# Kernel tuning notes

Hardware: AMD Instinct MI355X
Metric: run time of the kernel (lower is better)

Reference implementation:

```python
import jax, jax.numpy as jnp
import numpy as np

B, S, D, H, DH, R = 8, 2048, 1024, 16, 64, 32
ALPHA, BETA, GAMMA = 0.2, 0.1, 0.1


def setup_inputs() -> dict:
    key = jax.random.key(0)
    ks = jax.random.split(key, 5)
    x = jax.random.normal(ks[0], (B, S, D), jnp.float32)
    q = jax.random.normal(ks[1], (B, S, H, DH), jnp.float32)
    k = jax.random.normal(ks[2], (B, S, H, DH), jnp.float32)
    v_value = jax.random.normal(ks[3], (B, S, D), jnp.float32)
    # reentry_proj weight (orthogonal init approximated by scaled gaussian)
    W = jax.random.normal(ks[4], (D, D), jnp.float32) * np.float32(np.sqrt(0.5 / D))
    return {"x": x, "q": q, "k": k, "v_value": v_value, "W": W}


def _normalize(t):
    return t / (jnp.linalg.norm(t, axis=-1, keepdims=True) + 1e-6)


def reference(x, q, k, v_value, W):
    Bz, Sl, Dm = x.shape
    qf = q.reshape(Bz, Sl, Dm).transpose(1, 0, 2)        # (S, B, D)
    kf = k.reshape(Bz, Sl, Dm).transpose(1, 0, 2)        # (S, B, D)
    vf = v_value.transpose(1, 0, 2)                      # (S, B, D)
    U0 = jnp.zeros((Bz, R, Dm), x.dtype)
    V0 = jnp.zeros((Bz, R, Dm), x.dtype)

    def step(carry, inp):
        U, V = carry
        q_t, k_t, v_t = inp                              # each (B, D)
        U = (1.0 - ALPHA) * U + ALPHA * _normalize(q_t)[:, None, :]
        V = (1.0 - ALPHA) * V + ALPHA * _normalize(k_t)[:, None, :]
        # y_t = (U^T V) v_t, computed factorized: never materialize dim x dim
        s = jnp.einsum('brd,bd->br', V, v_t)             # (B, R)
        y = jnp.einsum('brd,br->bd', U, s)               # (B, D)
        n = jnp.maximum(jnp.linalg.norm(y, axis=-1, keepdims=True), 1e-6)
        y = y / (1.0 + BETA * (n - 1.0))                 # homeostasis
        fb = GAMMA * (y @ W.T)                           # reentry projection
        return (U, V), fb

    (_, _), fbs = jax.lax.scan(step, (U0, V0), (qf, kf, vf))
    return x + fbs.transpose(1, 0, 2)                    # (B, S, D)
```

## Files before the change

kernel.cpp:

```cpp
#include <hip/hip_runtime.h>
#include <hip/hip_bf16.h>
#include <cstdint>
#include <cstddef>

#define B_ 8
#define S_ 2048
#define D_ 1024
#define RFAC 32.0f
#define ALPHA 0.2f
#define BETA 0.1f
#define GAMMA 0.1f
#define KW 32
#define TB 64
#define PF_ 8

typedef float f32x4_t __attribute__((ext_vector_type(4)));
typedef short bf16x8_t __attribute__((ext_vector_type(8)));

__device__ __forceinline__ unsigned short f2bf(float f) {
    unsigned u = __float_as_uint(f);
    u = (u + 0x7fffu + ((u >> 16) & 1u)) >> 16;
    return (unsigned short)u;
}
__device__ __forceinline__ float bf2f(unsigned short h) {
    return __uint_as_float(((unsigned)h) << 16);
}

__global__ __launch_bounds__(256) void norms_k(const float* __restrict__ q,
                                               const float* __restrict__ k,
                                               float* __restrict__ rnq,
                                               float* __restrict__ rnk) {
    int row  = blockIdx.x * 4 + (threadIdx.x >> 6);
    int lane = threadIdx.x & 63;
    const float4* qr = (const float4*)(q + (size_t)row * D_);
    const float4* kr = (const float4*)(k + (size_t)row * D_);
    float sq = 0.f, sk = 0.f;
#pragma unroll
    for (int j = 0; j < 4; ++j) {
        float4 a = qr[lane + 64 * j];
        float4 b = kr[lane + 64 * j];
        sq += a.x * a.x + a.y * a.y + a.z * a.z + a.w * a.w;
        sk += b.x * b.x + b.y * b.y + b.z * b.z + b.w * b.w;
    }
#pragma unroll
    for (int off = 32; off > 0; off >>= 1) {
        sq += __shfl_xor(sq, off, 64);
        sk += __shfl_xor(sk, off, 64);
    }
    if (lane == 0) {
        rnq[row] = ALPHA / (sqrtf(sq) + 1e-6f);
        rnk[row] = ALPHA / (sqrtf(sk) + 1e-6f);
    }
}

__global__ __launch_bounds__(256) void wconv_k(const float* __restrict__ W,
                                               unsigned short* __restrict__ Wb) {
    int i = blockIdx.x * 256 + threadIdx.x;
    float4 w = ((const float4*)W)[i];
    ushort4 o;
    o.x = f2bf(w.x); o.y = f2bf(w.y); o.z = f2bf(w.z); o.w = f2bf(w.w);
    ((ushort4*)Wb)[i] = o;
}

__global__ __launch_bounds__(256) void ema_coef_k(const float* __restrict__ q,
                                                  const float* __restrict__ kk,
                                                  const float* __restrict__ rnq,
                                                  const float* __restrict__ rnk,
                                                  const float* __restrict__ vv,
                                                  unsigned short* __restrict__ Ub,
                                                  float* __restrict__ coef) {
    __shared__ float sm[TB * 8];
    const int chunks = S_ / TB;
    int b  = blockIdx.x / chunks;
    int t0 = (blockIdx.x % chunks) * TB;
    int ts = t0 - KW; if (ts < 0) ts = 0;
    int tid = threadIdx.x;
    int lane = tid & 63, wave = tid >> 6;
    size_t bbase = (size_t)b * S_ * D_ + tid * 4;
    const float* qp = q + bbase;
    const float* kp = kk + bbase;
    const float* vp = vv + bbase;
    unsigned short* up = Ub + bbase;
    const float* rq = rnq + b * S_;
    const float* rk = rnk + b * S_;

    float4 pq[PF_], pk[PF_], pv[PF_];
    float paq[PF_], pak[PF_];
#pragma unroll
    for (int j = 0; j < PF_; ++j) {
        size_t o = (size_t)(ts + j) * D_;
        pq[j] = *(const float4*)(qp + o);
        pk[j] = *(const float4*)(kp + o);
        paq[j] = rq[ts + j];
        pak[j] = rk[ts + j];
        if (ts + j >= t0) pv[j] = *(const float4*)(vp + o);
    }
    float u0 = 0.f, u1 = 0.f, u2 = 0.f, u3 = 0.f;
    float v0 = 0.f, v1 = 0.f, v2 = 0.f, v3 = 0.f;
    const float om = 1.f - ALPHA;
    const int NI = t0 + TB - ts;
    const int tend = t0 + TB;
    for (int g = 0; g < NI; g += PF_) {
#pragma unroll
        for (int j = 0; j < PF_; ++j) {
            int t = ts + g + j;
            float aq = paq[j], ak = pak[j];
            u0 = om * u0 + aq * pq[j].x; u1 = om * u1 + aq * pq[j].y;
            u2 = om * u2 + aq * pq[j].z; u3 = om * u3 + aq * pq[j].w;
            v0 = om * v0 + ak * pk[j].x; v1 = om * v1 + ak * pk[j].y;
            v2 = om * v2 + ak * pk[j].z; v3 = om * v3 + ak * pk[j].w;
            if (t >= t0) {
                float uu = u0 * u0 + u1 * u1 + u2 * u2 + u3 * u3;
                float sd = v0 * pv[j].x + v1 * pv[j].y + v2 * pv[j].z + v3 * pv[j].w;
#pragma unroll
                for (int off = 32; off > 0; off >>= 1) {
                    uu += __shfl_xor(uu, off, 64);
                    sd += __shfl_xor(sd, off, 64);
                }
                if (lane == 0) {
                    sm[(t - t0) * 8 + wave * 2 + 0] = uu;
                    sm[(t - t0) * 8 + wave * 2 + 1] = sd;
                }
                ushort4 us;
                us.x = f2bf(u0); us.y = f2bf(u1); us.z = f2bf(u2); us.w = f2bf(u3);
                *(ushort4*)(up + (size_t)t * D_) = us;
            }
            int tf = t + PF_;
            int tc = tf < tend ? tf : tend - 1;
            size_t o2 = (size_t)tc * D_;
            pq[j] = *(const float4*)(qp + o2);
            pk[j] = *(const float4*)(kp + o2);
            paq[j] = rq[tc];
            pak[j] = rk[tc];
            if (tf >= t0) pv[j] = *(const float4*)(vp + o2);
        }
    }
    __syncthreads();
    if (tid < TB) {
        float uu = sm[tid * 8 + 0] + sm[tid * 8 + 2] + sm[tid * 8 + 4] + sm[tid * 8 + 6];
        float sd = sm[tid * 8 + 1] + sm[tid * 8 + 3] + sm[tid * 8 + 5] + sm[tid * 8 + 7];
        float nrm = RFAC * fabsf(sd) * sqrtf(uu);
        float n = fmaxf(nrm, 1e-6f);
        coef[b * S_ + t0 + tid] = GAMMA * RFAC * sd / (1.f + BETA * (n - 1.f));
    }
}

#define BM 256
#define BN 256
#define BK 64
#define NT (D_ / BK)

__global__ __launch_bounds__(512, 2) void gemm_k(const unsigned short* __restrict__ A,
                                                 const unsigned short* __restrict__ Bw,
                                                 const float* __restrict__ coef,
                                                 const float* __restrict__ x,
                                                 float* __restrict__ out) {
    const int N = D_, K = D_;
    __shared__ unsigned short lds[2 * 2 * BM * BK];
    int bid = blockIdx.x;
    int swz = (bid & 7) * 32 + (bid >> 3);
    int tm = swz >> 2, tn = swz & 3;
    int m0 = tm * BM, n0 = tn * BN;
    int tid = threadIdx.x;
    int lane = tid & 63;
    int wid = tid >> 6;
    int wm = wid >> 2, wn = wid & 3;
    int lr = lane & 15, lg = lane >> 4;

    f32x4_t acc[8][4];
#pragma unroll
    for (int i = 0; i < 8; ++i)
#pragma unroll
        for (int j = 0; j < 4; ++j)
            acc[i][j] = (f32x4_t){0.f, 0.f, 0.f, 0.f};

#define STAGE_HALF(buf, kt, h)                                                        \
    {                                                                                 \
        int isB = (h) >> 1;                                                           \
        const unsigned short* Gp =                                                    \
            (isB ? Bw + (size_t)n0 * K : A + (size_t)m0 * K) + (size_t)(kt) * BK;     \
        unsigned short* Lp = lds + (buf) * 32768 + isB * 16384;                       \
        _Pragma("unroll")                                                             \
        for (int i = 0; i < 2; ++i) {                                                 \
            int c = i * 512 + tid;                \
            int row = ((h) & 1) * 128 + (c >> 3);                                     \
            int cl = c & 7;                                                           \
            int gc = cl ^ (row & 7);                   \
            __builtin_amdgcn_global_load_lds(                                         \
                (const __attribute__((address_space(1))) void*)(Gp + (size_t)row * K + gc * 8), \
                (__attribute__((address_space(3))) void*)((char*)Lp + (((((h)&1)*128 + (c>>3)) * 8 + cl) * 16)), \
                16, 0, 0);                                                            \
        }                                                                             \
    }
#define STAGE_TILE(buf, kt)                                                           \
    STAGE_HALF(buf, kt, 0); STAGE_HALF(buf, kt, 1);                                   \
    STAGE_HALF(buf, kt, 2); STAGE_HALF(buf, kt, 3);

    STAGE_TILE(0, 0);
    STAGE_TILE(1, 1);

    for (int t = 0; t < NT; ++t) {
        if (t == NT - 1) asm volatile("s_waitcnt vmcnt(0)" ::: "memory");
        else             asm volatile("s_waitcnt vmcnt(8)" ::: "memory");
        __builtin_amdgcn_s_barrier();
        const unsigned short* La = lds + (t & 1) * 32768;
        const unsigned short* Lb = La + 16384;
        bf16x8_t bfrag[4][2];
#pragma unroll
        for (int p = 0; p < 4; ++p) {
            if (p == 0) {
#pragma unroll
                for (int ni = 0; ni < 4; ++ni)
#pragma unroll
                    for (int kkk = 0; kkk < 2; ++kkk) {
                        int row = wn * 64 + ni * 16 + lr;
                        int ch = (kkk * 4 + lg) ^ (row & 7);
                        bfrag[ni][kkk] = *(const bf16x8_t*)(Lb + (row * 8 + ch) * 8);
                    }
            }
            bf16x8_t afrag[2][2];
#pragma unroll
            for (int qq = 0; qq < 2; ++qq)
#pragma unroll
                for (int kkk = 0; kkk < 2; ++kkk) {
                    int row = wm * 128 + p * 32 + qq * 16 + lr;
                    int ch = (kkk * 4 + lg) ^ (row & 7);
                    afrag[qq][kkk] = *(const bf16x8_t*)(La + (row * 8 + ch) * 8);
                }
            asm volatile("s_waitcnt lgkmcnt(0)" ::: "memory");
            __builtin_amdgcn_sched_barrier(0);
            __builtin_amdgcn_s_setprio(1);
#pragma unroll
            for (int qq = 0; qq < 2; ++qq)
#pragma unroll
                for (int ni = 0; ni < 4; ++ni)
#pragma unroll
                    for (int kkk = 0; kkk < 2; ++kkk)
                        acc[p * 2 + qq][ni] = __builtin_amdgcn_mfma_f32_16x16x32_bf16(
                            afrag[qq][kkk], bfrag[ni][kkk], acc[p * 2 + qq][ni], 0, 0, 0);
            __builtin_amdgcn_s_setprio(0);
            __builtin_amdgcn_s_barrier();
        }
        if (t + 2 < NT) { STAGE_TILE((t & 1), t + 2); }
    }
#undef STAGE_TILE
#undef STAGE_HALF

#pragma unroll
    for (int mi = 0; mi < 8; ++mi) {
#pragma unroll
        for (int i = 0; i < 4; ++i) {
            int m = m0 + wm * 128 + mi * 16 + lg * 4 + i;
            float cf = coef[m];
#pragma unroll
            for (int ni = 0; ni < 4; ++ni) {
                int n = n0 + wn * 64 + ni * 16 + lr;
                size_t idx = (size_t)m * N + n;
                out[idx] = x[idx] + cf * acc[mi][ni][i];
            }
        }
    }
}

extern "C" void kernel_launch(void* const* d_in, const int* in_sizes, int n_in,
                              void* d_out, int out_size, void* d_ws, size_t ws_size,
                              hipStream_t stream) {
    const float* x  = (const float*)d_in[0];
    const float* q  = (const float*)d_in[1];
    const float* k  = (const float*)d_in[2];
    const float* vv = (const float*)d_in[3];
    const float* W  = (const float*)d_in[4];
    float* out = (float*)d_out;

    const size_t M = (size_t)B_ * S_;
    char* ws = (char*)d_ws;
    unsigned short* Ub = (unsigned short*)ws;
    unsigned short* Wb = (unsigned short*)(ws + M * D_ * 2);
    float* coef = (float*)(ws + M * D_ * 2 + (size_t)D_ * D_ * 2);
    float* rnq  = coef + M;
    float* rnk  = rnq + M;
    size_t needed = M * D_ * 2 + (size_t)D_ * D_ * 2 + 3 * M * 4;
    if (ws_size < needed) return;

    norms_k<<<dim3(M / 4), dim3(256), 0, stream>>>(q, k, rnq, rnk);
    wconv_k<<<dim3((D_ * D_) / 1024), dim3(256), 0, stream>>>(W, Wb);
    ema_coef_k<<<dim3(B_ * (S_ / TB)), dim3(256), 0, stream>>>(q, k, rnq, rnk, vv, Ub, coef);
    gemm_k<<<dim3((M / BM) * (D_ / BN)), dim3(512), 0, stream>>>(Ub, Wb, coef, x, out);
}
```

Baseline: 129.4 us.

## Fuse row norms into EMA kernel and shrink GEMM tiles to 128x128

Removes the separate norms kernel by computing q/k row norms inside the EMA scan via wave shuffles plus a block-level LDS reduction with a __syncthreads per timestep. This saves one full read of q and k from global memory and one launch, but it adds a block barrier on every step of the serial recurrence, including the warm-up steps. The GEMM also moves from 256x256 tiles with 512 threads to 128x128 tiles with 256 threads and 4x4 accumulators per wave. That gives more blocks and lower register pressure, at the cost of less data reuse per tile.

```diff
diff --git a/kernel.cpp b/kernel.cpp
--- a/kernel.cpp
+++ b/kernel.cpp
@@ -26,33 +26,6 @@
     return __uint_as_float(((unsigned)h) << 16);
 }
 
-__global__ __launch_bounds__(256) void norms_k(const float* __restrict__ q,
-                                               const float* __restrict__ k,
-                                               float* __restrict__ rnq,
-                                               float* __restrict__ rnk) {
-    int row  = blockIdx.x * 4 + (threadIdx.x >> 6);
-    int lane = threadIdx.x & 63;
-    const float4* qr = (const float4*)(q + (size_t)row * D_);
-    const float4* kr = (const float4*)(k + (size_t)row * D_);
-    float sq = 0.f, sk = 0.f;
-#pragma unroll
-    for (int j = 0; j < 4; ++j) {
-        float4 a = qr[lane + 64 * j];
-        float4 b = kr[lane + 64 * j];
-        sq += a.x * a.x + a.y * a.y + a.z * a.z + a.w * a.w;
-        sk += b.x * b.x + b.y * b.y + b.z * b.z + b.w * b.w;
-    }
-#pragma unroll
-    for (int off = 32; off > 0; off >>= 1) {
-        sq += __shfl_xor(sq, off, 64);
-        sk += __shfl_xor(sk, off, 64);
-    }
-    if (lane == 0) {
-        rnq[row] = ALPHA / (sqrtf(sq) + 1e-6f);
-        rnk[row] = ALPHA / (sqrtf(sk) + 1e-6f);
-    }
-}
-
 __global__ __launch_bounds__(256) void wconv_k(const float* __restrict__ W,
                                                unsigned short* __restrict__ Wb) {
     int i = blockIdx.x * 256 + threadIdx.x;
@@ -62,14 +35,13 @@
     ((ushort4*)Wb)[i] = o;
 }
 
-__global__ __launch_bounds__(256) void ema_coef_k(const float* __restrict__ q,
-                                                  const float* __restrict__ kk,
-                                                  const float* __restrict__ rnq,
-                                                  const float* __restrict__ rnk,
-                                                  const float* __restrict__ vv,
-                                                  unsigned short* __restrict__ Ub,
-                                                  float* __restrict__ coef) {
-    __shared__ float sm[TB * 8];
+__global__ __launch_bounds__(256) void ema_fused_k(const float* __restrict__ q,
+                                                   const float* __restrict__ kk,
+                                                   const float* __restrict__ vv,
+                                                   unsigned short* __restrict__ Ub,
+                                                   float* __restrict__ coef) {
+    __shared__ float smn[2][8];
+    __shared__ float sm2[TB * 8];
     const int chunks = S_ / TB;
     int b  = blockIdx.x / chunks;
     int t0 = (blockIdx.x % chunks) * TB;
@@ -81,18 +53,13 @@
     const float* kp = kk + bbase;
     const float* vp = vv + bbase;
     unsigned short* up = Ub + bbase;
-    const float* rq = rnq + b * S_;
-    const float* rk = rnk + b * S_;
 
     float4 pq[PF_], pk[PF_], pv[PF_];
-    float paq[PF_], pak[PF_];
 #pragma unroll
     for (int j = 0; j < PF_; ++j) {
         size_t o = (size_t)(ts + j) * D_;
         pq[j] = *(const float4*)(qp + o);
         pk[j] = *(const float4*)(kp + o);
-        paq[j] = rq[ts + j];
-        pak[j] = rk[ts + j];
         if (ts + j >= t0) pv[j] = *(const float4*)(vp + o);
     }
     float u0 = 0.f, u1 = 0.f, u2 = 0.f, u3 = 0.f;
@@ -104,7 +71,25 @@
 #pragma unroll
         for (int j = 0; j < PF_; ++j) {
             int t = ts + g + j;
-            float aq = paq[j], ak = pak[j];
+            int slot = t & 1;
+            float sqq = pq[j].x * pq[j].x + pq[j].y * pq[j].y
+                      + pq[j].z * pq[j].z + pq[j].w * pq[j].w;
+            float sqk = pk[j].x * pk[j].x + pk[j].y * pk[j].y
+                      + pk[j].z * pk[j].z + pk[j].w * pk[j].w;
+#pragma unroll
+            for (int off = 32; off > 0; off >>= 1) {
+                sqq += __shfl_xor(sqq, off, 64);
+                sqk += __shfl_xor(sqk, off, 64);
+            }
+            if (lane == 0) {
+                smn[slot][wave * 2 + 0] = sqq;
+                smn[slot][wave * 2 + 1] = sqk;
+            }
+            __syncthreads();
+            float nq = smn[slot][0] + smn[slot][2] + smn[slot][4] + smn[slot][6];
+            float nk = smn[slot][1] + smn[slot][3] + smn[slot][5] + smn[slot][7];
+            float aq = ALPHA / (sqrtf(nq) + 1e-6f);
+            float ak = ALPHA / (sqrtf(nk) + 1e-6f);
             u0 = om * u0 + aq * pq[j].x; u1 = om * u1 + aq * pq[j].y;
             u2 = om * u2 + aq * pq[j].z; u3 = om * u3 + aq * pq[j].w;
             v0 = om * v0 + ak * pk[j].x; v1 = om * v1 + ak * pk[j].y;
@@ -118,8 +103,8 @@
                     sd += __shfl_xor(sd, off, 64);
                 }
                 if (lane == 0) {
-                    sm[(t - t0) * 8 + wave * 2 + 0] = uu;
-                    sm[(t - t0) * 8 + wave * 2 + 1] = sd;
+                    sm2[(t - t0) * 8 + wave * 2 + 0] = uu;
+                    sm2[(t - t0) * 8 + wave * 2 + 1] = sd;
                 }
                 ushort4 us;
                 us.x = f2bf(u0); us.y = f2bf(u1); us.z = f2bf(u2); us.w = f2bf(u3);
@@ -130,71 +115,64 @@
             size_t o2 = (size_t)tc * D_;
             pq[j] = *(const float4*)(qp + o2);
             pk[j] = *(const float4*)(kp + o2);
-            paq[j] = rq[tc];
-            pak[j] = rk[tc];
             if (tf >= t0) pv[j] = *(const float4*)(vp + o2);
         }
     }
     __syncthreads();
     if (tid < TB) {
-        float uu = sm[tid * 8 + 0] + sm[tid * 8 + 2] + sm[tid * 8 + 4] + sm[tid * 8 + 6];
-        float sd = sm[tid * 8 + 1] + sm[tid * 8 + 3] + sm[tid * 8 + 5] + sm[tid * 8 + 7];
+        float uu = sm2[tid * 8 + 0] + sm2[tid * 8 + 2] + sm2[tid * 8 + 4] + sm2[tid * 8 + 6];
+        float sd = sm2[tid * 8 + 1] + sm2[tid * 8 + 3] + sm2[tid * 8 + 5] + sm2[tid * 8 + 7];
         float nrm = RFAC * fabsf(sd) * sqrtf(uu);
         float n = fmaxf(nrm, 1e-6f);
         coef[b * S_ + t0 + tid] = GAMMA * RFAC * sd / (1.f + BETA * (n - 1.f));
     }
 }
 
-#define BM 256
-#define BN 256
+#define BM 128
+#define BN 128
 #define BK 64
 #define NT (D_ / BK)
 
-__global__ __launch_bounds__(512, 2) void gemm_k(const unsigned short* __restrict__ A,
-                                                 const unsigned short* __restrict__ Bw,
-                                                 const float* __restrict__ coef,
-                                                 const float* __restrict__ x,
-                                                 float* __restrict__ out) {
+__global__ __launch_bounds__(256) void gemm_k(const unsigned short* __restrict__ A,
+                                              const unsigned short* __restrict__ Bw,
+                                              const float* __restrict__ coef,
+                                              const float* __restrict__ x,
+                                              float* __restrict__ out) {
     const int N = D_, K = D_;
     __shared__ unsigned short lds[2 * 2 * BM * BK];
     int bid = blockIdx.x;
-    int swz = (bid & 7) * 32 + (bid >> 3);
-    int tm = swz >> 2, tn = swz & 3;
+    int swz = (bid & 7) * 128 + (bid >> 3);
+    int tm = swz >> 3, tn = swz & 7;
     int m0 = tm * BM, n0 = tn * BN;
     int tid = threadIdx.x;
     int lane = tid & 63;
     int wid = tid >> 6;
-    int wm = wid >> 2, wn = wid & 3;
+    int wr = wid >> 1, wc = wid & 1;
     int lr = lane & 15, lg = lane >> 4;
 
-    f32x4_t acc[8][4];
-#pragma unroll
-    for (int i = 0; i < 8; ++i)
+    f32x4_t acc[4][4];
+#pragma unroll
+    for (int i = 0; i < 4; ++i)
 #pragma unroll
         for (int j = 0; j < 4; ++j)
             acc[i][j] = (f32x4_t){0.f, 0.f, 0.f, 0.f};
 
-#define STAGE_HALF(buf, kt, h)                                                        \
+#define STAGE_MAT(buf, kt, isB)                                                       \
     {                                                                                 \
-        int isB = (h) >> 1;                                                           \
         const unsigned short* Gp =                                                    \
-            (isB ? Bw + (size_t)n0 * K : A + (size_t)m0 * K) + (size_t)(kt) * BK;     \
-        unsigned short* Lp = lds + (buf) * 32768 + isB * 16384;                       \
+            ((isB) ? Bw + (size_t)n0 * K : A + (size_t)m0 * K) + (size_t)(kt) * BK;   \
+        char* Lp = (char*)lds + (buf) * 32768 + (isB) * 16384;                        \
         _Pragma("unroll")                                                             \
-        for (int i = 0; i < 2; ++i) {                                                 \
-            int c = i * 512 + tid;                \
-            int row = ((h) & 1) * 128 + (c >> 3);                                     \
-            int cl = c & 7;                                                           \
+        for (int i = 0; i < 4; ++i) {                                                 \
+            int c = i * 256 + tid;                                                    \
+            int row = c >> 3, cl = c & 7;                                             \
             int gc = cl ^ (row & 7);                   \
             __builtin_amdgcn_global_load_lds(                                         \
                 (const __attribute__((address_space(1))) void*)(Gp + (size_t)row * K + gc * 8), \
-                (__attribute__((address_space(3))) void*)((char*)Lp + (((((h)&1)*128 + (c>>3)) * 8 + cl) * 16)), \
-                16, 0, 0);                                                            \
+                (__attribute__((address_space(3))) void*)(Lp + c * 16), 16, 0, 0);    \
         }                                                                             \
     }
-#define STAGE_TILE(buf, kt)                                                           \
-    STAGE_HALF(buf, kt, 0); STAGE_HALF(buf, kt, 1);                                   \
-    STAGE_HALF(buf, kt, 2); STAGE_HALF(buf, kt, 3);
+#define STAGE_TILE(buf, kt) STAGE_MAT(buf, kt, 0) STAGE_MAT(buf, kt, 1)
 
     STAGE_TILE(0, 0);
     STAGE_TILE(1, 1);
@@ -203,58 +181,51 @@
         if (t == NT - 1) asm volatile("s_waitcnt vmcnt(0)" ::: "memory");
         else             asm volatile("s_waitcnt vmcnt(8)" ::: "memory");
         __builtin_amdgcn_s_barrier();
-        const unsigned short* La = lds + (t & 1) * 32768;
-        const unsigned short* Lb = La + 16384;
-        bf16x8_t bfrag[4][2];
-#pragma unroll
-        for (int p = 0; p < 4; ++p) {
-            if (p == 0) {
+        const unsigned short* La = lds + (t & 1) * 16384;
+        const unsigned short* Lb = La + 8192;
+        bf16x8_t af[4][2], bf[4][2];
+#pragma unroll
+        for (int kkk = 0; kkk < 2; ++kkk) {
+#pragma unroll
+            for (int mi = 0; mi < 4; ++mi) {
+                int row = wr * 64 + mi * 16 + lr;
+                int ch = (kkk * 4 + lg) ^ (row & 7);
+                af[mi][kkk] = *(const bf16x8_t*)(La + (row * 8 + ch) * 8);
+            }
+#pragma unroll
+            for (int ni = 0; ni < 4; ++ni) {
+                int row = wc * 64 + ni * 16 + lr;
+                int ch = (kkk * 4 + lg) ^ (row & 7);
+                bf[ni][kkk] = *(const bf16x8_t*)(Lb + (row * 8 + ch) * 8);
+            }
+        }
+        asm volatile("s_waitcnt lgkmcnt(0)" ::: "memory");
+        __builtin_amdgcn_sched_barrier(0);
+        __builtin_amdgcn_s_setprio(1);
+#pragma unroll
+        for (int kkk = 0; kkk < 2; ++kkk)
+#pragma unroll
+            for (int mi = 0; mi < 4; ++mi)
 #pragma unroll
                 for (int ni = 0; ni < 4; ++ni)
-#pragma unroll
-                    for (int kkk = 0; kkk < 2; ++kkk) {
-                        int row = wn * 64 + ni * 16 + lr;
-                        int ch = (kkk * 4 + lg) ^ (row & 7);
-                        bfrag[ni][kkk] = *(const bf16x8_t*)(Lb + (row * 8 + ch) * 8);
-                    }
-            }
-            bf16x8_t afrag[2][2];
-#pragma unroll
-            for (int qq = 0; qq < 2; ++qq)
-#pragma unroll
-                for (int kkk = 0; kkk < 2; ++kkk) {
-                    int row = wm * 128 + p * 32 + qq * 16 + lr;
-                    int ch = (kkk * 4 + lg) ^ (row & 7);
-                    afrag[qq][kkk] = *(const bf16x8_t*)(La + (row * 8 + ch) * 8);
-                }
-            asm volatile("s_waitcnt lgkmcnt(0)" ::: "memory");
-            __builtin_amdgcn_sched_barrier(0);
-            __builtin_amdgcn_s_setprio(1);
-#pragma unroll
-            for (int qq = 0; qq < 2; ++qq)
-#pragma unroll
-                for (int ni = 0; ni < 4; ++ni)
-#pragma unroll
-                    for (int kkk = 0; kkk < 2; ++kkk)
-                        acc[p * 2 + qq][ni] = __builtin_amdgcn_mfma_f32_16x16x32_bf16(
-                            afrag[qq][kkk], bfrag[ni][kkk], acc[p * 2 + qq][ni], 0, 0, 0);
-            __builtin_amdgcn_s_setprio(0);
-            __builtin_amdgcn_s_barrier();
-        }
+                    acc[mi][ni] = __builtin_amdgcn_mfma_f32_16x16x32_bf16(
+                        af[mi][kkk], bf[ni][kkk], acc[mi][ni], 0, 0, 0);
+        __builtin_amdgcn_s_setprio(0);
+        __builtin_amdgcn_s_barrier();
         if (t + 2 < NT) { STAGE_TILE((t & 1), t + 2); }
     }
 #undef STAGE_TILE
-#undef STAGE_HALF
-
-#pragma unroll
-    for (int mi = 0; mi < 8; ++mi) {
+#undef STAGE_MAT
+
+#pragma unroll
+    for (int mi = 0; mi < 4; ++mi) {
 #pragma unroll
         for (int i = 0; i < 4; ++i) {
-            int m = m0 + wm * 128 + mi * 16 + lg * 4 + i;
+            int m = m0 + wr * 64 + mi * 16 + lg * 4 + i;
             float cf = coef[m];
 #pragma unroll
             for (int ni = 0; ni < 4; ++ni) {
-                int n = n0 + wn * 64 + ni * 16 + lr;
+                int n = n0 + wc * 64 + ni * 16 + lr;
                 size_t idx = (size_t)m * N + n;
                 out[idx] = x[idx] + cf * acc[mi][ni][i];
             }
@@ -277,13 +248,10 @@
     unsigned short* Ub = (unsigned short*)ws;
     unsigned short* Wb = (unsigned short*)(ws + M * D_ * 2);
     float* coef = (float*)(ws + M * D_ * 2 + (size_t)D_ * D_ * 2);
-    float* rnq  = coef + M;
-    float* rnk  = rnq + M;
-    size_t needed = M * D_ * 2 + (size_t)D_ * D_ * 2 + 3 * M * 4;
+    size_t needed = M * D_ * 2 + (size_t)D_ * D_ * 2 + M * 4;
     if (ws_size < needed) return;
 
-    norms_k<<<dim3(M / 4), dim3(256), 0, stream>>>(q, k, rnq, rnk);
     wconv_k<<<dim3((D_ * D_) / 1024), dim3(256), 0, stream>>>(W, Wb);
-    ema_coef_k<<<dim3(B_ * (S_ / TB)), dim3(256), 0, stream>>>(q, k, rnq, rnk, vv, Ub, coef);
-    gemm_k<<<dim3((M / BM) * (D_ / BN)), dim3(512), 0, stream>>>(Ub, Wb, coef, x, out);
-}
+    ema_fused_k<<<dim3(B_ * (S_ / TB)), dim3(256), 0, stream>>>(q, k, vv, Ub, coef);
+    gemm_k<<<dim3((M / BM) * (D_ / BN)), dim3(256), 0, stream>>>(Ub, Wb, coef, x, out);
+}
```

Measured after the change: 139.8 us. +8.0%, slower.
